# Performance work log

Hardware: AMD Instinct MI355X
Metric: run time of the kernel (lower is better)

## Reference

```python
import jax, jax.numpy as jnp
import numpy as np

N_NODES = 50000
N_EDGES = 800000
IN = 128
HID = 128
OUT = 128
EDGE_F = 2
EPS = 1e-30


def _linear_params(key, fan_in, fan_out, bias=True):
    k1, k2 = jax.random.split(key)
    bound = 1.0 / np.sqrt(fan_in)
    W = jax.random.uniform(k1, (fan_in, fan_out), jnp.float32, -bound, bound)
    if bias:
        b = jax.random.uniform(k2, (fan_out,), jnp.float32, -bound, bound)
        return W, b
    return (W,)


def setup_inputs() -> dict:
    key = jax.random.key(0)
    ks = jax.random.split(key, 12)
    node_feat = jax.random.normal(ks[0], (N_NODES, IN), jnp.float32)
    coord_feat = jax.random.normal(ks[1], (N_NODES, 3), jnp.float32)
    edge_feat = jax.random.normal(ks[2], (N_EDGES, EDGE_F), jnp.float32)
    src = jax.random.randint(ks[3], (N_EDGES,), 0, N_NODES, jnp.int32)
    dst = jax.random.randint(ks[4], (N_EDGES,), 0, N_NODES, jnp.int32)
    # edge_mlp: Linear(2*IN+EDGE_F+1 -> HID), SiLU, Linear(HID -> HID), SiLU
    eW1, eb1 = _linear_params(ks[5], 2 * IN + EDGE_F + 1, HID)
    eW2, eb2 = _linear_params(ks[6], HID, HID)
    # node_mlp: Linear(IN+HID -> HID), SiLU, Linear(HID -> OUT)
    nW1, nb1 = _linear_params(ks[7], IN + HID, HID)
    nW2, nb2 = _linear_params(ks[8], HID, OUT)
    # coord_mlp: Linear(HID -> HID), SiLU, Linear(HID -> 1, bias=False)
    cW1, cb1 = _linear_params(ks[9], HID, HID)
    (cW2,) = _linear_params(ks[10], HID, 1, bias=False)
    return {
        "node_feat": node_feat, "coord_feat": coord_feat, "edge_feat": edge_feat,
        "src": src, "dst": dst,
        "eW1": eW1, "eb1": eb1, "eW2": eW2, "eb2": eb2,
        "nW1": nW1, "nb1": nb1, "nW2": nW2, "nb2": nb2,
        "cW1": cW1, "cb1": cb1, "cW2": cW2,
    }


def reference(node_feat, coord_feat, edge_feat, src, dst,
              eW1, eb1, eW2, eb2, nW1, nb1, nW2, nb2, cW1, cb1, cW2):
    silu = jax.nn.silu
    n = node_feat.shape[0]
    # per-edge gathers (src -> dst message flow, as in DGL)
    h_src = node_feat[src]                      # [E, IN]
    h_dst = node_feat[dst]                      # [E, IN]
    x_diff = coord_feat[src] - coord_feat[dst]  # [E, 3]
    radial = jnp.sum(x_diff * x_diff, axis=1, keepdims=True)  # [E, 1]
    x_diff = x_diff / (jnp.sqrt(radial) + EPS)
    # edge MLP
    f = jnp.concatenate([h_src, h_dst, radial, edge_feat], axis=-1)  # [E, 2*IN+1+EF]
    msg_h = silu(silu(f @ eW1 + eb1) @ eW2 + eb2)                    # [E, HID]
    msg_x = (silu(msg_h @ cW1 + cb1) @ cW2) * x_diff                 # [E, 3]
    # scatter to destination nodes: sum for h, mean for x
    h_neigh = jax.ops.segment_sum(msg_h, dst, num_segments=n)        # [N, HID]
    x_sum = jax.ops.segment_sum(msg_x, dst, num_segments=n)          # [N, 3]
    deg = jax.ops.segment_sum(jnp.ones((msg_x.shape[0],), msg_x.dtype), dst, num_segments=n)
    x_neigh = x_sum / jnp.maximum(deg, 1.0)[:, None]
    # node update
    h = silu(jnp.concatenate([node_feat, h_neigh], axis=-1) @ nW1 + nb1) @ nW2 + nb2
    x = coord_feat + x_neigh
    return h, x
```

## Files before the change

### kernel.cpp

```cpp
#include <hip/hip_runtime.h>
#include <hip/hip_bf16.h>

#define N_NODES 50000
#define E_TOTAL 800000
#define IN      128
#define HID     128
#define EPB     64
#define XOFF    ((size_t)N_NODES * HID)
#define FP      296
#define H1OFF   160
#define HP      136
#define CP      264

typedef __attribute__((ext_vector_type(8))) short short8v;
typedef __attribute__((ext_vector_type(4))) float f32x4;

__device__ __forceinline__ float silu_f(float x) { return x / (1.0f + __expf(-x)); }

__device__ __forceinline__ uint pkbf(float lo, float hi) {
    float2 f; f.x = lo; f.y = hi;
    __hip_bfloat162 h = __float22bfloat162_rn(f);
    union { __hip_bfloat162 h; uint u; } c; c.h = h;
    return c.u;
}

__device__ __forceinline__ ushort f2bf(float x) {
    uint u = __float_as_uint(x);
    u += 0x7fff + ((u >> 16) & 1);
    return (ushort)(u >> 16);
}

__global__ __launch_bounds__(256) void prep_kernel(
    const float* __restrict__ eW1, const float* __restrict__ eW2,
    const float* __restrict__ cW1, const float* __restrict__ nW1,
    const float* __restrict__ nW2, const float* __restrict__ node_feat,
    ushort* __restrict__ pk1, ushort* __restrict__ pk2, ushort* __restrict__ pk3,
    ushort* __restrict__ pkn1, ushort* __restrict__ pkn2,
    ushort* __restrict__ nfb, int do_nfb)
{
    int id = blockIdx.x * 256 + threadIdx.x;
    if (id < 14848) {
        const float* W; ushort* dp; int K, idx;
        if (id < 4608)       { idx = id;         W = eW1; dp = pk1;  K = 259; }
        else if (id < 6656)  { idx = id - 4608;  W = eW2; dp = pk2;  K = 128; }
        else if (id < 8704)  { idx = id - 6656;  W = cW1; dp = pk3;  K = 128; }
        else if (id < 12800) { idx = id - 8704;  W = nW1; dp = pkn1; K = 256; }
        else                 { idx = id - 12800; W = nW2; dp = pkn2; K = 128; }
        int kt = idx >> 9, n = (idx >> 6) & 7, ll = idx & 63;
        int col = (n << 4) + (ll & 15);
        short8v o;
#pragma unroll
        for (int j = 0; j < 8; ++j) {
            int k = (kt << 5) + ((ll >> 4) << 3) + j;
            o[j] = (k < K) ? (short)f2bf(W[(size_t)k * 128 + col]) : (short)0;
        }
        *reinterpret_cast<short8v*>(dp + (size_t)idx * 8) = o;
    } else if (do_nfb) {
        int idx = id - 14848;
        if (idx < N_NODES * 16) {
            const float4* s = reinterpret_cast<const float4*>(node_feat + (size_t)idx * 8);
            float4 a = s[0], b = s[1];
            uint4 u;
            u.x = pkbf(a.x, a.y); u.y = pkbf(a.z, a.w);
            u.z = pkbf(b.x, b.y); u.w = pkbf(b.z, b.w);
            *reinterpret_cast<uint4*>(nfb + (size_t)idx * 8) = u;
        }
    }
}

__global__ __launch_bounds__(256) void hist_kernel(
    const int* __restrict__ dst, int* __restrict__ cnt)
{
    int e = blockIdx.x * 256 + threadIdx.x;
    if (e < E_TOTAL) atomicAdd(&cnt[dst[e]], 1);
}

__global__ __launch_bounds__(1024) void scan_kernel(
    int* __restrict__ ptr, int* __restrict__ ptr2)
{
    __shared__ int wsum[16];
    __shared__ int carry_s;
    const int t = threadIdx.x, lane = t & 63, wv = t >> 6;
    if (t == 0) carry_s = 0;
    __syncthreads();
    for (int base = 0; base < N_NODES; base += 1024) {
        int v = (base + t < N_NODES) ? ptr[base + t] : 0;
        int x = v;
#pragma unroll
        for (int off = 1; off < 64; off <<= 1) {
            int y = __shfl_up(x, off);
            if (lane >= off) x += y;
        }
        if (lane == 63) wsum[wv] = x;
        __syncthreads();
        if (wv == 0) {
            int s = (lane < 16) ? wsum[lane] : 0;
#pragma unroll
            for (int off = 1; off < 16; off <<= 1) {
                int y = __shfl_up(s, off);
                if (lane >= off) s += y;
            }
            if (lane < 16) wsum[lane] = s;
        }
        __syncthreads();
        int wbase = (wv == 0) ? 0 : wsum[wv - 1];
        int excl = carry_s + wbase + x - v;
        if (base + t < N_NODES) { ptr[base + t] = excl; ptr2[base + t] = excl; }
        __syncthreads();
        if (t == 1023) carry_s += wsum[15];
        __syncthreads();
    }
    if (t == 0) { ptr[N_NODES] = E_TOTAL; ptr2[N_NODES] = E_TOTAL; }
}

__global__ __launch_bounds__(256) void scatter_kernel(
    const int* __restrict__ dst, int* __restrict__ ptr2, int* __restrict__ perm)
{
    int e = blockIdx.x * 256 + threadIdx.x;
    if (e < E_TOTAL) {
        int p = atomicAdd(&ptr2[dst[e]], 1);
        perm[p] = e;
    }
}

template<bool NFB>
__global__ __launch_bounds__(512, 8) void edge_kernel(
    const float* __restrict__ node_feat, const ushort* __restrict__ nfb,
    const float* __restrict__ coord, const float* __restrict__ edge_feat,
    const int* __restrict__ src, const int* __restrict__ dst,
    const int* __restrict__ perm, int use_perm,
    const ushort* __restrict__ pk1, const ushort* __restrict__ pk2,
    const ushort* __restrict__ pk3,
    const float* __restrict__ eb1, const float* __restrict__ eb2,
    const float* __restrict__ cb1, const float* __restrict__ cW2,
    float* __restrict__ hacc, float* __restrict__ xacc)
{
    __shared__ __attribute__((aligned(16))) ushort fbuf[EPB][FP];
    __shared__ int   sbuf[EPB], dbuf[EPB];
    __shared__ float xdbuf[EPB][4];
    __shared__ float pbuf[4][EPB];

    const int t   = threadIdx.x;
    const int l   = t & 63;
    const int w   = t >> 6;
    const int ch  = w & 3;
    const int eh  = w >> 2;
    const int r16 = l & 15;
    const int g   = l >> 4;
    const int e_base = blockIdx.x * EPB;

    int ee = 0;
    if (t < EPB) {
        ee = use_perm ? perm[e_base + t] : (e_base + t);
        sbuf[t] = src[ee];
        dbuf[t] = dst[ee];
    }
    __syncthreads();

    {
        const int e = t >> 3;
        const int c = (t & 7) << 5;
        if (NFB) {
            const ushort* sp = (c < 128) ? nfb + (size_t)sbuf[e] * 128 + c
                                         : nfb + (size_t)dbuf[e] * 128 + (c - 128);
            const short8v* spv = reinterpret_cast<const short8v*>(sp);
#pragma unroll
            for (int i = 0; i < 4; ++i)
                *reinterpret_cast<short8v*>(&fbuf[e][c + (i << 3)]) = spv[i];
        } else {
            const float* sp = (c < 128) ? node_feat + (size_t)sbuf[e] * 128 + c
                                        : node_feat + (size_t)dbuf[e] * 128 + (c - 128);
            const float4* spv = reinterpret_cast<const float4*>(sp);
#pragma unroll
            for (int i = 0; i < 4; ++i) {
                float4 a = spv[2 * i], b = spv[2 * i + 1];
                uint4 u;
                u.x = pkbf(a.x, a.y); u.y = pkbf(a.z, a.w);
                u.z = pkbf(b.x, b.y); u.w = pkbf(b.z, b.w);
                *reinterpret_cast<uint4*>(&fbuf[e][c + (i << 3)]) = u;
            }
        }
    }
    if (t < EPB) {
        const int e = t, s = sbuf[e], d = dbuf[e];
        float dx = coord[(size_t)s*3+0] - coord[(size_t)d*3+0];
        float dy = coord[(size_t)s*3+1] - coord[(size_t)d*3+1];
        float dz = coord[(size_t)s*3+2] - coord[(size_t)d*3+2];
        float radial = dx*dx + dy*dy + dz*dz;
        float inv = 1.0f / (sqrtf(radial) + 1e-30f);
        fbuf[e][256] = f2bf(radial);
        fbuf[e][257] = f2bf(edge_feat[(size_t)ee*2 + 0]);
        fbuf[e][258] = f2bf(edge_feat[(size_t)ee*2 + 1]);
#pragma unroll
        for (int k = 259; k < 288; ++k) fbuf[e][k] = 0;
        xdbuf[e][0] = dx * inv; xdbuf[e][1] = dy * inv; xdbuf[e][2] = dz * inv;
    }
    __syncthreads();

    const f32x4 zero = {0.f, 0.f, 0.f, 0.f};
    const short8v* pkv1 = reinterpret_cast<const short8v*>(pk1);
    const short8v* pkv2 = reinterpret_cast<const short8v*>(pk2);
    const short8v* pkv3 = reinterpret_cast<const short8v*>(pk3);

    f32x4 acc[2][2];
    acc[0][0] = zero; acc[0][1] = zero; acc[1][0] = zero; acc[1][1] = zero;
    for (int kt = 0; kt < 9; ++kt) {
        short8v b0 = *reinterpret_cast<const short8v*>(&fbuf[(eh << 5) + r16][(kt << 5) + (g << 3)]);
        short8v b1 = *reinterpret_cast<const short8v*>(&fbuf[(eh << 5) + 16 + r16][(kt << 5) + (g << 3)]);
#pragma unroll
        for (int nt = 0; nt < 2; ++nt) {
            short8v a = pkv1[(((kt << 3) + (ch << 1) + nt) << 6) + l];
            acc[0][nt] = __builtin_amdgcn_mfma_f32_16x16x32_bf16(a, b0, acc[0][nt], 0, 0, 0);
            acc[1][nt] = __builtin_amdgcn_mfma_f32_16x16x32_bf16(a, b1, acc[1][nt], 0, 0, 0);
        }
    }
    __syncthreads();
#pragma unroll
    for (int nt = 0; nt < 2; ++nt) {
        int cb = (ch << 5) + (nt << 4) + (g << 2);
        float4 bias = *reinterpret_cast<const float4*>(&eb1[cb]);
#pragma unroll
        for (int et = 0; et < 2; ++et) {
            int e = (eh << 5) + (et << 4) + r16;
            f32x4 v = acc[et][nt];
            uint2 p;
            p.x = pkbf(silu_f(v[0] + bias.x), silu_f(v[1] + bias.y));
            p.y = pkbf(silu_f(v[2] + bias.z), silu_f(v[3] + bias.w));
            *reinterpret_cast<uint2*>(&fbuf[e][H1OFF + cb]) = p;
        }
    }
    __syncthreads();

    acc[0][0] = zero; acc[0][1] = zero; acc[1][0] = zero; acc[1][1] = zero;
    for (int kt = 0; kt < 4; ++kt) {
        short8v b0 = *reinterpret_cast<const short8v*>(&fbuf[(eh << 5) + r16][H1OFF + (kt << 5) + (g << 3)]);
        short8v b1 = *reinterpret_cast<const short8v*>(&fbuf[(eh << 5) + 16 + r16][H1OFF + (kt << 5) + (g << 3)]);
#pragma unroll
        for (int nt = 0; nt < 2; ++nt) {
            short8v a = pkv2[(((kt << 3) + (ch << 1) + nt) << 6) + l];
            acc[0][nt] = __builtin_amdgcn_mfma_f32_16x16x32_bf16(a, b0, acc[0][nt], 0, 0, 0);
            acc[1][nt] = __builtin_amdgcn_mfma_f32_16x16x32_bf16(a, b1, acc[1][nt], 0, 0, 0);
        }
    }
#pragma unroll
    for (int nt = 0; nt < 2; ++nt) {
        int cb = (ch << 5) + (nt << 4) + (g << 2);
        float4 bias = *reinterpret_cast<const float4*>(&eb2[cb]);
#pragma unroll
        for (int et = 0; et < 2; ++et) {
            int e = (eh << 5) + (et << 4) + r16;
            f32x4 v = acc[et][nt];
            uint2 p;
            p.x = pkbf(silu_f(v[0] + bias.x), silu_f(v[1] + bias.y));
            p.y = pkbf(silu_f(v[2] + bias.z), silu_f(v[3] + bias.w));
            *reinterpret_cast<uint2*>(&fbuf[e][cb]) = p;
        }
    }
    __syncthreads();

    {
        const int c = t & 127;
        const int q = t >> 7;
        float sum = 0.f;
        int cur = dbuf[q << 4];
#pragma unroll
        for (int i = 0; i < 16; ++i) {
            int e = (q << 4) + i;
            sum += __uint_as_float((uint)fbuf[e][c] << 16);
            int nxt = (i < 15) ? dbuf[e + 1] : -1;
            if (nxt != cur) {
                atomicAdd(&hacc[(size_t)cur * HID + c], sum);
                sum = 0.f; cur = nxt;
            }
        }
    }

    acc[0][0] = zero; acc[0][1] = zero; acc[1][0] = zero; acc[1][1] = zero;
    for (int kt = 0; kt < 4; ++kt) {
        short8v b0 = *reinterpret_cast<const short8v*>(&fbuf[(eh << 5) + r16][(kt << 5) + (g << 3)]);
        short8v b1 = *reinterpret_cast<const short8v*>(&fbuf[(eh << 5) + 16 + r16][(kt << 5) + (g << 3)]);
#pragma unroll
        for (int nt = 0; nt < 2; ++nt) {
            short8v a = pkv3[(((kt << 3) + (ch << 1) + nt) << 6) + l];
            acc[0][nt] = __builtin_amdgcn_mfma_f32_16x16x32_bf16(a, b0, acc[0][nt], 0, 0, 0);
            acc[1][nt] = __builtin_amdgcn_mfma_f32_16x16x32_bf16(a, b1, acc[1][nt], 0, 0, 0);
        }
    }
    float part[2] = {0.f, 0.f};
#pragma unroll
    for (int nt = 0; nt < 2; ++nt) {
        int cb = (ch << 5) + (nt << 4) + (g << 2);
        float4 bias = *reinterpret_cast<const float4*>(&cb1[cb]);
        float4 cw   = *reinterpret_cast<const float4*>(&cW2[cb]);
#pragma unroll
        for (int et = 0; et < 2; ++et) {
            f32x4 v = acc[et][nt];
            part[et] += silu_f(v[0] + bias.x) * cw.x + silu_f(v[1] + bias.y) * cw.y
                      + silu_f(v[2] + bias.z) * cw.z + silu_f(v[3] + bias.w) * cw.w;
        }
    }
#pragma unroll
    for (int et = 0; et < 2; ++et) {
        part[et] += __shfl_xor(part[et], 16);
        part[et] += __shfl_xor(part[et], 32);
    }
    if (l < 16) {
        pbuf[ch][(eh << 5) + r16]      = part[0];
        pbuf[ch][(eh << 5) + 16 + r16] = part[1];
    }
    __syncthreads();

    if (t < EPB) {
        float s = pbuf[0][t] + pbuf[1][t] + pbuf[2][t] + pbuf[3][t];
        int gd = dbuf[t];
        atomicAdd(&xacc[(size_t)gd*3 + 0], s * xdbuf[t][0]);
        atomicAdd(&xacc[(size_t)gd*3 + 1], s * xdbuf[t][1]);
        atomicAdd(&xacc[(size_t)gd*3 + 2], s * xdbuf[t][2]);
    }
}

template<bool NFB>
__global__ __launch_bounds__(256) void node_kernel(
    const float* __restrict__ node_feat, const ushort* __restrict__ nfb,
    const float* __restrict__ coord,
    const ushort* __restrict__ pkn1, const ushort* __restrict__ pkn2,
    const float* __restrict__ nb1, const float* __restrict__ nb2,
    float* __restrict__ dout, const int* __restrict__ ptr)
{
    __shared__ __attribute__((aligned(16))) ushort catb[32][CP];
    __shared__ __attribute__((aligned(16))) ushort h1b[32][HP];

    const int t   = threadIdx.x;
    const int l   = t & 63;
    const int w   = t >> 6;
    const int ch  = w & 1;
    const int eh  = w >> 1;
    const int r16 = l & 15;
    const int g   = l >> 4;
    const int nb  = blockIdx.x * 32;

    {
        int nd = t >> 3;
        int c  = (t & 7) << 5;
        int gn = nb + nd; if (gn >= N_NODES) gn = N_NODES - 1;
        if (c < 128) {
            if (NFB) {
                const short8v* spv = reinterpret_cast<const short8v*>(nfb + (size_t)gn * 128 + c);
#pragma unroll
                for (int i = 0; i < 4; ++i)
                    *reinterpret_cast<short8v*>(&catb[nd][c + (i << 3)]) = spv[i];
            } else {
                const float4* spv = reinterpret_cast<const float4*>(node_feat + (size_t)gn * 128 + c);
#pragma unroll
                for (int i = 0; i < 4; ++i) {
                    float4 a = spv[2 * i], b = spv[2 * i + 1];
                    uint4 u;
                    u.x = pkbf(a.x, a.y); u.y = pkbf(a.z, a.w);
                    u.z = pkbf(b.x, b.y); u.w = pkbf(b.z, b.w);
                    *reinterpret_cast<uint4*>(&catb[nd][c + (i << 3)]) = u;
                }
            }
        } else {
            const float4* spv = reinterpret_cast<const float4*>(dout + (size_t)gn * HID + (c - 128));
#pragma unroll
            for (int i = 0; i < 4; ++i) {
                float4 a = spv[2 * i], b = spv[2 * i + 1];
                uint4 u;
                u.x = pkbf(a.x, a.y); u.y = pkbf(a.z, a.w);
                u.z = pkbf(b.x, b.y); u.w = pkbf(b.z, b.w);
                *reinterpret_cast<uint4*>(&catb[nd][c + (i << 3)]) = u;
            }
        }
    }
    __syncthreads();

    const f32x4 zero = {0.f, 0.f, 0.f, 0.f};
    const short8v* pv1 = reinterpret_cast<const short8v*>(pkn1);
    const short8v* pv2 = reinterpret_cast<const short8v*>(pkn2);

    f32x4 acc[4];
#pragma unroll
    for (int nt = 0; nt < 4; ++nt) acc[nt] = zero;
    for (int kt = 0; kt < 8; ++kt) {
        short8v b = *reinterpret_cast<const short8v*>(&catb[(eh << 4) + r16][(kt << 5) + (g << 3)]);
#pragma unroll
        for (int nt = 0; nt < 4; ++nt) {
            short8v a = pv1[(((kt << 3) + (ch << 2) + nt) << 6) + l];
            acc[nt] = __builtin_amdgcn_mfma_f32_16x16x32_bf16(a, b, acc[nt], 0, 0, 0);
        }
    }
#pragma unroll
    for (int nt = 0; nt < 4; ++nt) {
        int cb = (ch << 6) + (nt << 4) + (g << 2);
        float4 bias = *reinterpret_cast<const float4*>(&nb1[cb]);
        int nd = (eh << 4) + r16;
        f32x4 v = acc[nt];
        uint2 p;
        p.x = pkbf(silu_f(v[0] + bias.x), silu_f(v[1] + bias.y));
        p.y = pkbf(silu_f(v[2] + bias.z), silu_f(v[3] + bias.w));
        *reinterpret_cast<uint2*>(&h1b[nd][cb]) = p;
    }
    __syncthreads();

#pragma unroll
    for (int nt = 0; nt < 4; ++nt) acc[nt] = zero;
    for (int kt = 0; kt < 4; ++kt) {
        short8v b = *reinterpret_cast<const short8v*>(&h1b[(eh << 4) + r16][(kt << 5) + (g << 3)]);
#pragma unroll
        for (int nt = 0; nt < 4; ++nt) {
            short8v a = pv2[(((kt << 3) + (ch << 2) + nt) << 6) + l];
            acc[nt] = __builtin_amdgcn_mfma_f32_16x16x32_bf16(a, b, acc[nt], 0, 0, 0);
        }
    }
    {
        int gw = nb + (eh << 4) + r16;
        if (gw < N_NODES) {
#pragma unroll
            for (int nt = 0; nt < 4; ++nt) {
                int cb = (ch << 6) + (nt << 4) + (g << 2);
                float4 bias = *reinterpret_cast<const float4*>(&nb2[cb]);
                f32x4 v = acc[nt];
                float4 o;
                o.x = v[0] + bias.x; o.y = v[1] + bias.y;
                o.z = v[2] + bias.z; o.w = v[3] + bias.w;
                *reinterpret_cast<float4*>(&dout[(size_t)gw * HID + cb]) = o;
            }
        }
    }

    if (t < 96) {
        int nd = t / 3, d = t - 3 * nd;
        int gn = nb + nd;
        if (gn < N_NODES) {
            size_t xi = XOFF + (size_t)gn * 3 + d;
            float dg = (float)(ptr[gn + 1] - ptr[gn]);
            dg = dg > 1.0f ? dg : 1.0f;
            dout[xi] = coord[(size_t)gn * 3 + d] + dout[xi] / dg;
        }
    }
}

extern "C" void kernel_launch(void* const* d_in, const int* in_sizes, int n_in,
                              void* d_out, int out_size, void* d_ws, size_t ws_size,
                              hipStream_t stream) {
    const float* node_feat = (const float*)d_in[0];
    const float* coord     = (const float*)d_in[1];
    const float* edge_feat = (const float*)d_in[2];
    const int*   src       = (const int*)d_in[3];
    const int*   dst       = (const int*)d_in[4];
    const float* eW1 = (const float*)d_in[5];
    const float* eb1 = (const float*)d_in[6];
    const float* eW2 = (const float*)d_in[7];
    const float* eb2 = (const float*)d_in[8];
    const float* nW1 = (const float*)d_in[9];
    const float* nb1 = (const float*)d_in[10];
    const float* nW2 = (const float*)d_in[11];
    const float* nb2 = (const float*)d_in[12];
    const float* cW1 = (const float*)d_in[13];
    const float* cb1 = (const float*)d_in[14];
    const float* cW2 = (const float*)d_in[15];

    float* out = (float*)d_out;
    char* base = (char*)d_ws;
    int*    ptrb = (int*)base;
    int*    ptr2 = (int*)(base + 200064);
    ushort* pk1  = (ushort*)(base + 400128);
    ushort* pk2  = (ushort*)(base + 473856);
    ushort* pk3  = (ushort*)(base + 506624);
    ushort* pkn1 = (ushort*)(base + 539392);
    ushort* pkn2 = (ushort*)(base + 604928);
    int*    perm = (int*)(base + 637696);
    ushort* nfb  = (ushort*)(base + 3837696);
    const bool use_perm = ws_size >= 3837696;
    const bool use_nfb  = ws_size >= 16637696;

    hipMemsetAsync(d_out, 0, (size_t)out_size * sizeof(float), stream);
    hipMemsetAsync(d_ws, 0, 200064, stream);

    int prep_grid = use_nfb ? (14848 + N_NODES * 16 + 255) / 256 : 58;
    prep_kernel<<<prep_grid, 256, 0, stream>>>(
        eW1, eW2, cW1, nW1, nW2, node_feat,
        pk1, pk2, pk3, pkn1, pkn2, nfb, use_nfb ? 1 : 0);

    hist_kernel<<<(E_TOTAL + 255) / 256, 256, 0, stream>>>(dst, ptrb);
    scan_kernel<<<1, 1024, 0, stream>>>(ptrb, ptr2);
    if (use_perm)
        scatter_kernel<<<(E_TOTAL + 255) / 256, 256, 0, stream>>>(dst, ptr2, perm);

    if (use_nfb) {
        edge_kernel<true><<<E_TOTAL / EPB, 512, 0, stream>>>(
            node_feat, nfb, coord, edge_feat, src, dst, perm, use_perm ? 1 : 0,
            pk1, pk2, pk3, eb1, eb2, cb1, cW2, out, out + XOFF);
        node_kernel<true><<<(N_NODES + 31) / 32, 256, 0, stream>>>(
            node_feat, nfb, coord, pkn1, pkn2, nb1, nb2, out, ptrb);
    } else {
        edge_kernel<false><<<E_TOTAL / EPB, 512, 0, stream>>>(
            node_feat, nfb, coord, edge_feat, src, dst, perm, use_perm ? 1 : 0,
            pk1, pk2, pk3, eb1, eb2, cb1, cW2, out, out + XOFF);
        node_kernel<false><<<(N_NODES + 31) / 32, 256, 0, stream>>>(
            node_feat, nfb, coord, pkn1, pkn2, nb1, nb2, out, ptrb);
    }
}
```

Before: 553.7 us.

## Precompute per-node first-layer projections and gather them per edge

Splits the first edge-MLP layer algebraically. The src and dst halves of eW1 are applied once per node by a new MFMA kernel that writes a bf16 table of size N×256. The edge kernel then gathers two 128-wide rows and adds the radial, edge-feature and bias terms on scalar lanes, which removes the K=259 GEMM from every edge. The single-block scan is also replaced by a three-kernel multi-block scan. This costs an extra 25.6MB workspace table and adds bf16 rounding of the precomputed projections.

After: 523.6 us, median of 2. -5.4%, faster.

```diff
diff --git a/kernel.cpp b/kernel.cpp
--- a/kernel.cpp
+++ b/kernel.cpp
@@ -30,22 +30,30 @@
     return (ushort)(u >> 16);
 }
 
+__device__ __forceinline__ float bf2f(short s) {
+    return __uint_as_float(((uint)(ushort)s) << 16);
+}
+
 __global__ __launch_bounds__(256) void prep_kernel(
     const float* __restrict__ eW1, const float* __restrict__ eW2,
     const float* __restrict__ cW1, const float* __restrict__ nW1,
-    const float* __restrict__ nW2, const float* __restrict__ node_feat,
-    ushort* __restrict__ pk1, ushort* __restrict__ pk2, ushort* __restrict__ pk3,
+    const float* __restrict__ nW2, const float* __restrict__ eb1,
+    const float* __restrict__ node_feat,
+    ushort* __restrict__ pk1old, ushort* __restrict__ pka, ushort* __restrict__ pkb,
+    ushort* __restrict__ pk2, ushort* __restrict__ pk3,
     ushort* __restrict__ pkn1, ushort* __restrict__ pkn2,
-    ushort* __restrict__ nfb, int do_nfb)
+    float* __restrict__ cmb, ushort* __restrict__ nfb, int do_nfb)
 {
     int id = blockIdx.x * 256 + threadIdx.x;
-    if (id < 14848) {
+    if (id < 18944) {
         const float* W; ushort* dp; int K, idx;
-        if (id < 4608)       { idx = id;         W = eW1; dp = pk1;  K = 259; }
-        else if (id < 6656)  { idx = id - 4608;  W = eW2; dp = pk2;  K = 128; }
-        else if (id < 8704)  { idx = id - 6656;  W = cW1; dp = pk3;  K = 128; }
-        else if (id < 12800) { idx = id - 8704;  W = nW1; dp = pkn1; K = 256; }
-        else                 { idx = id - 12800; W = nW2; dp = pkn2; K = 128; }
+        if (id < 4608)       { idx = id;         W = eW1;            dp = pk1old; K = 259; }
+        else if (id < 6656)  { idx = id - 4608;  W = eW1;            dp = pka;    K = 128; }
+        else if (id < 8704)  { idx = id - 6656;  W = eW1 + 128*128;  dp = pkb;    K = 128; }
+        else if (id < 10752) { idx = id - 8704;  W = eW2;            dp = pk2;    K = 128; }
+        else if (id < 12800) { idx = id - 10752; W = cW1;            dp = pk3;    K = 128; }
+        else if (id < 16896) { idx = id - 12800; W = nW1;            dp = pkn1;   K = 256; }
+        else                 { idx = id - 16896; W = nW2;            dp = pkn2;   K = 128; }
         int kt = idx >> 9, n = (idx >> 6) & 7, ll = idx & 63;
         int col = (n << 4) + (ll & 15);
         short8v o;
@@ -55,8 +63,14 @@
             o[j] = (k < K) ? (short)f2bf(W[(size_t)k * 128 + col]) : (short)0;
         }
         *reinterpret_cast<short8v*>(dp + (size_t)idx * 8) = o;
+    } else if (id < 19072) {
+        int c = id - 18944;
+        cmb[c*4+0] = eW1[256*128 + c];
+        cmb[c*4+1] = eW1[257*128 + c];
+        cmb[c*4+2] = eW1[258*128 + c];
+        cmb[c*4+3] = eb1[c];
     } else if (do_nfb) {
-        int idx = id - 14848;
+        int idx = id - 19072;
         if (idx < N_NODES * 16) {
             const float4* s = reinterpret_cast<const float4*>(node_feat + (size_t)idx * 8);
             float4 a = s[0], b = s[1];
@@ -75,42 +89,66 @@
     if (e < E_TOTAL) atomicAdd(&cnt[dst[e]], 1);
 }
 
-__global__ __launch_bounds__(1024) void scan_kernel(
-    int* __restrict__ ptr, int* __restrict__ ptr2)
-{
-    __shared__ int wsum[16];
-    __shared__ int carry_s;
-    const int t = threadIdx.x, lane = t & 63, wv = t >> 6;
-    if (t == 0) carry_s = 0;
-    __syncthreads();
-    for (int base = 0; base < N_NODES; base += 1024) {
-        int v = (base + t < N_NODES) ? ptr[base + t] : 0;
-        int x = v;
-#pragma unroll
-        for (int off = 1; off < 64; off <<= 1) {
-            int y = __shfl_up(x, off);
-            if (lane >= off) x += y;
-        }
-        if (lane == 63) wsum[wv] = x;
-        __syncthreads();
-        if (wv == 0) {
-            int s = (lane < 16) ? wsum[lane] : 0;
-#pragma unroll
-            for (int off = 1; off < 16; off <<= 1) {
-                int y = __shfl_up(s, off);
-                if (lane >= off) s += y;
-            }
-            if (lane < 16) wsum[lane] = s;
-        }
-        __syncthreads();
-        int wbase = (wv == 0) ? 0 : wsum[wv - 1];
-        int excl = carry_s + wbase + x - v;
-        if (base + t < N_NODES) { ptr[base + t] = excl; ptr2[base + t] = excl; }
-        __syncthreads();
-        if (t == 1023) carry_s += wsum[15];
-        __syncthreads();
-    }
-    if (t == 0) { ptr[N_NODES] = E_TOTAL; ptr2[N_NODES] = E_TOTAL; }
+__global__ __launch_bounds__(1024) void scan_a(
+    const int* __restrict__ cnt, int* __restrict__ part)
+{
+    __shared__ int ws[16];
+    int t = threadIdx.x, lane = t & 63, wv = t >> 6;
+    int i = blockIdx.x * 1024 + t;
+    int v = (i < N_NODES) ? cnt[i] : 0;
+#pragma unroll
+    for (int off = 32; off >= 1; off >>= 1) v += __shfl_xor(v, off);
+    if (lane == 0) ws[wv] = v;
+    __syncthreads();
+    if (t < 16) {
+        int s = ws[t];
+#pragma unroll
+        for (int off = 8; off >= 1; off >>= 1) s += __shfl_xor(s, off);
+        if (t == 0) part[blockIdx.x] = s;
+    }
+}
+
+__global__ __launch_bounds__(64) void scan_b(int* __restrict__ part, int n)
+{
+    int t = threadIdx.x;
+    int v = (t < n) ? part[t] : 0;
+    int x = v;
+#pragma unroll
+    for (int off = 1; off < 64; off <<= 1) {
+        int y = __shfl_up(x, off);
+        if (t >= off) x += y;
+    }
+    if (t < n) part[t] = x - v;
+}
+
+__global__ __launch_bounds__(1024) void scan_c(
+    int* __restrict__ cnt, const int* __restrict__ part, int* __restrict__ ptr2)
+{
+    __shared__ int ws[16];
+    int t = threadIdx.x, lane = t & 63, wv = t >> 6;
+    int i = blockIdx.x * 1024 + t;
+    int v = (i < N_NODES) ? cnt[i] : 0;
+    int x = v;
+#pragma unroll
+    for (int off = 1; off < 64; off <<= 1) {
+        int y = __shfl_up(x, off);
+        if (lane >= off) x += y;
+    }
+    if (lane == 63) ws[wv] = x;
+    __syncthreads();
+    if (t < 16) {
+        int s = ws[t], xx = s;
+#pragma unroll
+        for (int off = 1; off < 16; off <<= 1) {
+            int y = __shfl_up(xx, off);
+            if (t >= off) xx += y;
+        }
+        ws[t] = xx - s;
+    }
+    __syncthreads();
+    int excl = part[blockIdx.x] + ws[wv] + x - v;
+    if (i < N_NODES) { cnt[i] = excl; ptr2[i] = excl; }
+    if (i == N_NODES - 1) { cnt[N_NODES] = E_TOTAL; ptr2[N_NODES] = E_TOTAL; }
 }
 
 __global__ __launch_bounds__(256) void scatter_kernel(
@@ -120,6 +158,242 @@
     if (e < E_TOTAL) {
         int p = atomicAdd(&ptr2[dst[e]], 1);
         perm[p] = e;
+    }
+}
+
+__global__ __launch_bounds__(256) void ygemm_kernel(
+    const float* __restrict__ node_feat,
+    const ushort* __restrict__ pka, const ushort* __restrict__ pkb,
+    ushort* __restrict__ y)
+{
+    __shared__ __attribute__((aligned(16))) ushort catb[32][HP];
+    __shared__ __attribute__((aligned(16))) ushort ybuf[32][CP];
+
+    const int t   = threadIdx.x;
+    const int l   = t & 63;
+    const int ch  = t >> 6;
+    const int r16 = l & 15;
+    const int g   = l >> 4;
+    const int nb  = blockIdx.x * 32;
+
+    {
+        int nd = t >> 3;
+        int c  = (t & 7) << 4;
+        int gn = nb + nd; if (gn >= N_NODES) gn = N_NODES - 1;
+        const float4* sp = reinterpret_cast<const float4*>(node_feat + (size_t)gn * 128 + c);
+        float4 a = sp[0], b = sp[1], cc = sp[2], dd = sp[3];
+        uint4 u0, u1;
+        u0.x = pkbf(a.x, a.y);  u0.y = pkbf(a.z, a.w);
+        u0.z = pkbf(b.x, b.y);  u0.w = pkbf(b.z, b.w);
+        u1.x = pkbf(cc.x, cc.y); u1.y = pkbf(cc.z, cc.w);
+        u1.z = pkbf(dd.x, dd.y); u1.w = pkbf(dd.z, dd.w);
+        *reinterpret_cast<uint4*>(&catb[nd][c])     = u0;
+        *reinterpret_cast<uint4*>(&catb[nd][c + 8]) = u1;
+    }
+    __syncthreads();
+
+    const f32x4 zero = {0.f, 0.f, 0.f, 0.f};
+    const short8v* pa = reinterpret_cast<const short8v*>((ch < 2) ? pka : pkb);
+    const int nbase = (ch & 1) << 2;
+
+    f32x4 acc[2][4];
+#pragma unroll
+    for (int et = 0; et < 2; ++et)
+#pragma unroll
+        for (int nt = 0; nt < 4; ++nt) acc[et][nt] = zero;
+
+    for (int kt = 0; kt < 4; ++kt) {
+        short8v b0 = *reinterpret_cast<const short8v*>(&catb[r16][(kt << 5) + (g << 3)]);
+        short8v b1 = *reinterpret_cast<const short8v*>(&catb[16 + r16][(kt << 5) + (g << 3)]);
+#pragma unroll
+        for (int nt = 0; nt < 4; ++nt) {
+            short8v a = pa[(((kt << 3) + nbase + nt) << 6) + l];
+            acc[0][nt] = __builtin_amdgcn_mfma_f32_16x16x32_bf16(a, b0, acc[0][nt], 0, 0, 0);
+            acc[1][nt] = __builtin_amdgcn_mfma_f32_16x16x32_bf16(a, b1, acc[1][nt], 0, 0, 0);
+        }
+    }
+#pragma unroll
+    for (int nt = 0; nt < 4; ++nt) {
+        int cb = (ch << 6) + (nt << 4) + (g << 2);
+#pragma unroll
+        for (int et = 0; et < 2; ++et) {
+            f32x4 v = acc[et][nt];
+            uint2 p;
+            p.x = pkbf(v[0], v[1]); p.y = pkbf(v[2], v[3]);
+            *reinterpret_cast<uint2*>(&ybuf[(et << 4) + r16][cb]) = p;
+        }
+    }
+    __syncthreads();
+
+#pragma unroll
+    for (int i = 0; i < 4; ++i) {
+        int idx = t + (i << 8);
+        int nd  = idx >> 5;
+        int c16 = (idx & 31) << 3;
+        int gn  = nb + nd;
+        if (gn < N_NODES)
+            *reinterpret_cast<short8v*>(y + (size_t)gn * 256 + c16) =
+                *reinterpret_cast<const short8v*>(&ybuf[nd][c16]);
+    }
+}
+
+__global__ __launch_bounds__(512, 4) void edge2_kernel(
+    const ushort* __restrict__ y, const float* __restrict__ coord,
+    const float* __restrict__ edge_feat,
+    const int* __restrict__ src, const int* __restrict__ dst,
+    const int* __restrict__ perm,
+    const float* __restrict__ cmb,
+    const ushort* __restrict__ pk2, const ushort* __restrict__ pk3,
+    const float* __restrict__ eb2,
+    const float* __restrict__ cb1, const float* __restrict__ cW2,
+    float* __restrict__ hacc, float* __restrict__ xacc)
+{
+    __shared__ __attribute__((aligned(16))) ushort h1buf[EPB][HP];
+    __shared__ __attribute__((aligned(16))) ushort msgbuf[EPB][HP];
+    __shared__ int   sbuf[EPB], dbuf[EPB];
+    __shared__ float xdbuf[EPB][4];
+    __shared__ float rbuf[EPB][4];
+    __shared__ float pbuf[4][EPB];
+
+    const int t   = threadIdx.x;
+    const int l   = t & 63;
+    const int w   = t >> 6;
+    const int ch  = w & 3;
+    const int eh  = w >> 2;
+    const int r16 = l & 15;
+    const int g   = l >> 4;
+    const int e_base = blockIdx.x * EPB;
+
+    if (t < EPB) {
+        int ee = perm[e_base + t];
+        int s = src[ee], d = dst[ee];
+        sbuf[t] = s; dbuf[t] = d;
+        float dx = coord[(size_t)s*3+0] - coord[(size_t)d*3+0];
+        float dy = coord[(size_t)s*3+1] - coord[(size_t)d*3+1];
+        float dz = coord[(size_t)s*3+2] - coord[(size_t)d*3+2];
+        float radial = dx*dx + dy*dy + dz*dz;
+        float inv = 1.0f / (sqrtf(radial) + 1e-30f);
+        xdbuf[t][0] = dx * inv; xdbuf[t][1] = dy * inv; xdbuf[t][2] = dz * inv;
+        rbuf[t][0] = radial;
+        rbuf[t][1] = edge_feat[(size_t)ee*2 + 0];
+        rbuf[t][2] = edge_feat[(size_t)ee*2 + 1];
+    }
+    __syncthreads();
+
+    {
+        const int c = (t & 15) << 3;
+        const float4* cmb4 = reinterpret_cast<const float4*>(cmb);
+#pragma unroll
+        for (int p = 0; p < 2; ++p) {
+            int e = (t >> 4) + (p << 5);
+            short8v a8 = *reinterpret_cast<const short8v*>(y + (size_t)sbuf[e] * 256 + c);
+            short8v b8 = *reinterpret_cast<const short8v*>(y + (size_t)dbuf[e] * 256 + 128 + c);
+            float r = rbuf[e][0], f0 = rbuf[e][1], f1 = rbuf[e][2];
+            float vv[8];
+#pragma unroll
+            for (int j = 0; j < 8; ++j) {
+                float4 q = cmb4[c + j];
+                float s = bf2f(a8[j]) + bf2f(b8[j]) + r*q.x + f0*q.y + f1*q.z + q.w;
+                vv[j] = silu_f(s);
+            }
+            uint4 u;
+            u.x = pkbf(vv[0], vv[1]); u.y = pkbf(vv[2], vv[3]);
+            u.z = pkbf(vv[4], vv[5]); u.w = pkbf(vv[6], vv[7]);
+            *reinterpret_cast<uint4*>(&h1buf[e][c]) = u;
+        }
+    }
+    __syncthreads();
+
+    const f32x4 zero = {0.f, 0.f, 0.f, 0.f};
+    const short8v* pkv2 = reinterpret_cast<const short8v*>(pk2);
+    const short8v* pkv3 = reinterpret_cast<const short8v*>(pk3);
+
+    f32x4 acc[2][2];
+    acc[0][0] = zero; acc[0][1] = zero; acc[1][0] = zero; acc[1][1] = zero;
+    for (int kt = 0; kt < 4; ++kt) {
+        short8v b0 = *reinterpret_cast<const short8v*>(&h1buf[(eh << 5) + r16][(kt << 5) + (g << 3)]);
+        short8v b1 = *reinterpret_cast<const short8v*>(&h1buf[(eh << 5) + 16 + r16][(kt << 5) + (g << 3)]);
+#pragma unroll
+        for (int nt = 0; nt < 2; ++nt) {
+            short8v a = pkv2[(((kt << 3) + (ch << 1) + nt) << 6) + l];
+            acc[0][nt] = __builtin_amdgcn_mfma_f32_16x16x32_bf16(a, b0, acc[0][nt], 0, 0, 0);
+            acc[1][nt] = __builtin_amdgcn_mfma_f32_16x16x32_bf16(a, b1, acc[1][nt], 0, 0, 0);
+        }
+    }
+#pragma unroll
+    for (int nt = 0; nt < 2; ++nt) {
+        int cb = (ch << 5) + (nt << 4) + (g << 2);
+        float4 bias = *reinterpret_cast<const float4*>(&eb2[cb]);
+#pragma unroll
+        for (int et = 0; et < 2; ++et) {
+            int e = (eh << 5) + (et << 4) + r16;
+            f32x4 v = acc[et][nt];
+            uint2 p;
+            p.x = pkbf(silu_f(v[0] + bias.x), silu_f(v[1] + bias.y));
+            p.y = pkbf(silu_f(v[2] + bias.z), silu_f(v[3] + bias.w));
+            *reinterpret_cast<uint2*>(&msgbuf[e][cb]) = p;
+        }
+    }
+    __syncthreads();
+
+    {
+        const int c = t & 127;
+        const int q = t >> 7;
+        float sum = 0.f;
+        int cur = dbuf[q << 4];
+#pragma unroll
+        for (int i = 0; i < 16; ++i) {
+            int e = (q << 4) + i;
+            sum += __uint_as_float((uint)msgbuf[e][c] << 16);
+            int nxt = (i < 15) ? dbuf[e + 1] : -1;
+            if (nxt != cur) {
+                atomicAdd(&hacc[(size_t)cur * HID + c], sum);
+                sum = 0.f; cur = nxt;
+            }
+        }
+    }
+
+    acc[0][0] = zero; acc[0][1] = zero; acc[1][0] = zero; acc[1][1] = zero;
+    for (int kt = 0; kt < 4; ++kt) {
+        short8v b0 = *reinterpret_cast<const short8v*>(&msgbuf[(eh << 5) + r16][(kt << 5) + (g << 3)]);
+        short8v b1 = *reinterpret_cast<const short8v*>(&msgbuf[(eh << 5) + 16 + r16][(kt << 5) + (g << 3)]);
+#pragma unroll
+        for (int nt = 0; nt < 2; ++nt) {
+            short8v a = pkv3[(((kt << 3) + (ch << 1) + nt) << 6) + l];
+            acc[0][nt] = __builtin_amdgcn_mfma_f32_16x16x32_bf16(a, b0, acc[0][nt], 0, 0, 0);
+            acc[1][nt] = __builtin_amdgcn_mfma_f32_16x16x32_bf16(a, b1, acc[1][nt], 0, 0, 0);
+        }
+    }
+    float part[2] = {0.f, 0.f};
+#pragma unroll
+    for (int nt = 0; nt < 2; ++nt) {
+        int cb = (ch << 5) + (nt << 4) + (g << 2);
+        float4 bias = *reinterpret_cast<const float4*>(&cb1[cb]);
+        float4 cw   = *reinterpret_cast<const float4*>(&cW2[cb]);
+#pragma unroll
+        for (int et = 0; et < 2; ++et) {
+            f32x4 v = acc[et][nt];
+            part[et] += silu_f(v[0] + bias.x) * cw.x + silu_f(v[1] + bias.y) * cw.y
+                      + silu_f(v[2] + bias.z) * cw.z + silu_f(v[3] + bias.w) * cw.w;
+        }
+    }
+#pragma unroll
+    for (int et = 0; et < 2; ++et) {
+        part[et] += __shfl_xor(part[et], 16);
+        part[et] += __shfl_xor(part[et], 32);
+    }
+    if (l < 16) {
+        pbuf[ch][(eh << 5) + r16]      = part[0];
+        pbuf[ch][(eh << 5) + 16 + r16] = part[1];
+    }
+    __syncthreads();
+
+    if (t < EPB) {
+        float s = pbuf[0][t] + pbuf[1][t] + pbuf[2][t] + pbuf[3][t];
+        int gd = dbuf[t];
+        atomicAdd(&xacc[(size_t)gd*3 + 0], s * xdbuf[t][0]);
+        atomicAdd(&xacc[(size_t)gd*3 + 1], s * xdbuf[t][1]);
+        atomicAdd(&xacc[(size_t)gd*3 + 2], s * xdbuf[t][2]);
     }
 }
 
@@ -462,42 +736,59 @@
 
     float* out = (float*)d_out;
     char* base = (char*)d_ws;
-    int*    ptrb = (int*)base;
-    int*    ptr2 = (int*)(base + 200064);
-    ushort* pk1  = (ushort*)(base + 400128);
-    ushort* pk2  = (ushort*)(base + 473856);
-    ushort* pk3  = (ushort*)(base + 506624);
-    ushort* pkn1 = (ushort*)(base + 539392);
-    ushort* pkn2 = (ushort*)(base + 604928);
-    int*    perm = (int*)(base + 637696);
-    ushort* nfb  = (ushort*)(base + 3837696);
-    const bool use_perm = ws_size >= 3837696;
-    const bool use_nfb  = ws_size >= 16637696;
+    int*    ptrb   = (int*)base;
+    int*    part   = (int*)(base + 200064);
+    int*    ptr2   = (int*)(base + 200320);
+    ushort* pk1old = (ushort*)(base + 400384);
+    ushort* pka    = (ushort*)(base + 474112);
+    ushort* pkb    = (ushort*)(base + 506880);
+    ushort* pk2    = (ushort*)(base + 539648);
+    ushort* pk3    = (ushort*)(base + 572416);
+    ushort* pkn1   = (ushort*)(base + 605184);
+    ushort* pkn2   = (ushort*)(base + 670720);
+    float*  cmb    = (float*)(base + 703488);
+    int*    perm   = (int*)(base + 705536);
+    ushort* ybuf   = (ushort*)(base + 3905536);
+    const size_t need_y    = 3905536 + (size_t)N_NODES * 256 * 2;
+    const size_t need_nfb  = 3905536 + (size_t)N_NODES * 128 * 2;
+    const size_t need_perm = 3905536;
+    const bool use_y    = ws_size >= need_y;
+    const bool use_nfb  = !use_y && ws_size >= need_nfb;
+    const bool use_perm = ws_size >= need_perm;
 
     hipMemsetAsync(d_out, 0, (size_t)out_size * sizeof(float), stream);
     hipMemsetAsync(d_ws, 0, 200064, stream);
 
-    int prep_grid = use_nfb ? (14848 + N_NODES * 16 + 255) / 256 : 58;
+    int prep_grid = (use_nfb ? (19072 + N_NODES * 16) + 255 : 19072 + 255) / 256;
     prep_kernel<<<prep_grid, 256, 0, stream>>>(
-        eW1, eW2, cW1, nW1, nW2, node_feat,
-        pk1, pk2, pk3, pkn1, pkn2, nfb, use_nfb ? 1 : 0);
+        eW1, eW2, cW1, nW1, nW2, eb1, node_feat,
+        pk1old, pka, pkb, pk2, pk3, pkn1, pkn2, cmb, ybuf, use_nfb ? 1 : 0);
 
     hist_kernel<<<(E_TOTAL + 255) / 256, 256, 0, stream>>>(dst, ptrb);
-    scan_kernel<<<1, 1024, 0, stream>>>(ptrb, ptr2);
+    scan_a<<<49, 1024, 0, stream>>>(ptrb, part);
+    scan_b<<<1, 64, 0, stream>>>(part, 49);
+    scan_c<<<49, 1024, 0, stream>>>(ptrb, part, ptr2);
     if (use_perm)
         scatter_kernel<<<(E_TOTAL + 255) / 256, 256, 0, stream>>>(dst, ptr2, perm);
 
-    if (use_nfb) {
+    if (use_y) {
+        ygemm_kernel<<<(N_NODES + 31) / 32, 256, 0, stream>>>(node_feat, pka, pkb, ybuf);
+        edge2_kernel<<<E_TOTAL / EPB, 512, 0, stream>>>(
+            ybuf, coord, edge_feat, src, dst, perm, cmb,
+            pk2, pk3, eb2, cb1, cW2, out, out + XOFF);
+        node_kernel<false><<<(N_NODES + 31) / 32, 256, 0, stream>>>(
+            node_feat, ybuf, coord, pkn1, pkn2, nb1, nb2, out, ptrb);
+    } else if (use_nfb) {
         edge_kernel<true><<<E_TOTAL / EPB, 512, 0, stream>>>(
-            node_feat, nfb, coord, edge_feat, src, dst, perm, use_perm ? 1 : 0,
-            pk1, pk2, pk3, eb1, eb2, cb1, cW2, out, out + XOFF);
+            node_feat, ybuf, coord, edge_feat, src, dst, perm, use_perm ? 1 : 0,
+            pk1old, pk2, pk3, eb1, eb2, cb1, cW2, out, out + XOFF);
         node_kernel<true><<<(N_NODES + 31) / 32, 256, 0, stream>>>(
-            node_feat, nfb, coord, pkn1, pkn2, nb1, nb2, out, ptrb);
+            node_feat, ybuf, coord, pkn1, pkn2, nb1, nb2, out, ptrb);
     } else {
         edge_kernel<false><<<E_TOTAL / EPB, 512, 0, stream>>>(
-            node_feat, nfb, coord, edge_feat, src, dst, perm, use_perm ? 1 : 0,
-            pk1, pk2, pk3, eb1, eb2, cb1, cW2, out, out + XOFF);
+            node_feat, ybuf, coord, edge_feat, src, dst, perm, use_perm ? 1 : 0,
+            pk1old, pk2, pk3, eb1, eb2, cb1, cW2, out, out + XOFF);
         node_kernel<false><<<(N_NODES + 31) / 32, 256, 0, stream>>>(
-            node_feat, nfb, coord, pkn1, pkn2, nb1, nb2, out, ptrb);
-    }
-}
+            node_feat, ybuf, coord, pkn1, pkn2, nb1, nb2, out, ptrb);
+    }
+}
```
